# Performance work log

Hardware: AMD Instinct MI355X
Metric: run time of the kernel (lower is better)

Reference implementation:

```python
import jax, jax.numpy as jnp
import numpy as np

B, R, C, H = 2048, 100, 64, 256  # batch graphs, regions/graph, in_channels, hidden
N = B * R                         # total nodes
E = 3276800                       # edges


def setup_inputs() -> dict:
    key = jax.random.key(0)
    ks = jax.random.split(key, 12)
    state = jax.random.normal(ks[0], (N, C), dtype=jnp.float32)
    edge_index = jax.random.randint(ks[1], (2, E), 0, N, dtype=jnp.int64)
    action = jax.random.uniform(ks[2], (B, R, R), dtype=jnp.float32)
    s = lambda f: 1.0 / np.sqrt(f)
    W_gcn = jax.random.uniform(ks[3], (C, C), jnp.float32, -s(C), s(C))
    b_gcn = jnp.zeros((C,), jnp.float32)
    W1 = jax.random.uniform(ks[4], (C + R, H), jnp.float32, -s(C + R), s(C + R))
    b1 = jax.random.uniform(ks[5], (H,), jnp.float32, -s(C + R), s(C + R))
    W2 = jax.random.uniform(ks[6], (H, H), jnp.float32, -s(H), s(H))
    b2 = jax.random.uniform(ks[7], (H,), jnp.float32, -s(H), s(H))
    W3 = jax.random.uniform(ks[8], (H, 1), jnp.float32, -s(H), s(H))
    b3 = jax.random.uniform(ks[9], (1,), jnp.float32, -s(H), s(H))
    return {"state": state, "edge_index": edge_index, "action": action,
            "W_gcn": W_gcn, "b_gcn": b_gcn, "W1": W1, "b1": b1,
            "W2": W2, "b2": b2, "W3": W3, "b3": b3}


def gcn_conv(x, edge_index, W, b):
    # PyG GCNConv: add self-loops, symmetric degree normalization, then aggregate.
    n = x.shape[0]
    loops = jnp.arange(n, dtype=edge_index.dtype)
    src = jnp.concatenate([edge_index[0], loops])
    dst = jnp.concatenate([edge_index[1], loops])
    deg = jax.ops.segment_sum(jnp.ones_like(dst, dtype=x.dtype), dst, num_segments=n)
    dinv = deg ** -0.5  # deg >= 1 thanks to self-loops
    xw = x @ W
    msg = xw[src] * (dinv[src] * dinv[dst])[:, None]
    return jax.ops.segment_sum(msg, dst, num_segments=n) + b


def reference(state, edge_index, action, W_gcn, b_gcn, W1, b1, W2, b2, W3, b3):
    out = jax.nn.relu(gcn_conv(state, edge_index, W_gcn, b_gcn))
    x = out + state                              # residual, [N, C]
    x = x.reshape(-1, R, C)                      # [B, R, C]
    concat = jnp.concatenate([x, action], axis=-1)  # [B, R, C+R]
    x = jax.nn.relu(concat @ W1 + b1)
    x = jax.nn.relu(x @ W2 + b2)
    x = jnp.sum(x, axis=1)                       # sum pooling over regions -> [B, H]
    return (x @ W3 + b3).squeeze(-1)             # [B]
```

## Files before the change

### kernel.cpp

```cpp
#include <hip/hip_runtime.h>
#include <hip/hip_bf16.h>
#include <cstdint>
#include <cstddef>

#define N_NODES 204800
#define N_EDGES 3276800
#define NB 2048
#define NR 100
#define NC 64
#define NH 256
#define KPAD 192
#define NBKT 400

typedef __attribute__((ext_vector_type(8))) short short8;
typedef __attribute__((ext_vector_type(4))) float f32x4;
typedef unsigned int uint32;

__device__ __forceinline__ void gload16(const void* g, void* l) {
    __builtin_amdgcn_global_load_lds(
        (const __attribute__((address_space(1))) uint32_t*)(g),
        (__attribute__((address_space(3))) uint32_t*)(l), 16, 0, 0);
}

__device__ __forceinline__ ushort f2bf(float v) {
    __hip_bfloat16 h = __float2bfloat16(v);
    return *reinterpret_cast<ushort*>(&h);
}

__device__ __forceinline__ uint32 pack2bf(float a, float b) {
    return (uint32)f2bf(a) | ((uint32)f2bf(b) << 16);
}

__device__ __forceinline__ float bflo(uint32 v) { return __uint_as_float(v << 16); }
__device__ __forceinline__ float bfhi(uint32 v) { return __uint_as_float(v & 0xFFFF0000u); }


__global__ __launch_bounds__(256) void k_bhist(const int* __restrict__ ei,
                                               int* __restrict__ bcnt) {
    __shared__ int h[NBKT];
    int t = threadIdx.x;
    for (int i = t; i < NBKT; i += 256) h[i] = 0;
    __syncthreads();
    #pragma unroll 16
    for (int k = 0; k < 16; ++k) {
        int e = blockIdx.x * 4096 + k * 256 + t;
        atomicAdd(&h[ei[N_EDGES + e] >> 9], 1);
    }
    __syncthreads();
    for (int i = t; i < NBKT; i += 256)
        if (h[i]) atomicAdd(&bcnt[i], h[i]);
}

__global__ void k_bscan(const int* __restrict__ bcnt, int* __restrict__ boffs,
                        int* __restrict__ bcur) {
    __shared__ int tmp[512];
    int t = threadIdx.x;
    int v = (t < NBKT) ? bcnt[t] : 0;
    tmp[t] = v;
    __syncthreads();
    for (int off = 1; off < 512; off <<= 1) {
        int x = 0;
        if (t >= off) x = tmp[t - off];
        __syncthreads();
        tmp[t] += x;
        __syncthreads();
    }
    if (t < NBKT) {
        int o = tmp[t] - v;
        boffs[t] = o;
        bcur[t] = o;
    }
}

__global__ __launch_bounds__(256) void k_bscat(const int* __restrict__ ei,
                                               int* __restrict__ bcur,
                                               uint32* __restrict__ part) {
    __shared__ int hist[NBKT];
    __shared__ int curb[NBKT];
    int tid = threadIdx.x;
    for (int i = tid; i < NBKT; i += 256) hist[i] = 0;
    __syncthreads();
    #pragma unroll 16
    for (int k = 0; k < 16; ++k) {
        int e = blockIdx.x * 4096 + k * 256 + tid;
        atomicAdd(&hist[ei[N_EDGES + e] >> 9], 1);
    }
    __syncthreads();
    for (int i = tid; i < NBKT; i += 256) {
        int c = hist[i];
        curb[i] = c ? atomicAdd(&bcur[i], c) : 0;
    }
    __syncthreads();
    #pragma unroll 16
    for (int k = 0; k < 16; ++k) {
        int e = blockIdx.x * 4096 + k * 256 + tid;
        int s = ei[e];
        int d = ei[N_EDGES + e];
        int b = d >> 9;
        int p = atomicAdd(&curb[b], 1);
        part[p] = (uint32)s | ((uint32)(d & 511) << 18);
    }
}

__global__ __launch_bounds__(512) void k_sortb(
    const uint32* __restrict__ part, const int* __restrict__ boffs,
    const int* __restrict__ bcnt, int* __restrict__ csr,
    int* __restrict__ cnt, int* __restrict__ offs, float* __restrict__ dinv,
    const float* __restrict__ state, uint32* __restrict__ ssb32) {
    __shared__ int h[512];
    __shared__ int cur[512];
    __shared__ float sdv[512];
    int b = blockIdx.x, t = threadIdx.x;
    h[t] = 0;
    __syncthreads();
    int base = boffs[b], n = bcnt[b];
    for (int i = t; i < n; i += 512)
        atomicAdd(&h[part[base + i] >> 18], 1);
    __syncthreads();
    int v = h[t];
    int node = b * 512 + t;
    cnt[node] = v;
    float dv = rsqrtf((float)(v + 1));
    dinv[node] = dv;
    sdv[t] = dv;
    __syncthreads();
    for (int off = 1; off < 512; off <<= 1) {
        int x = 0;
        if (t >= off) x = h[t - off];
        __syncthreads();
        h[t] += x;
        __syncthreads();
    }
    int excl = h[t] - v;
    offs[node] = base + excl;
    cur[t] = excl;
    __syncthreads();
    for (int i = t; i < n; i += 512) {
        uint32 ew = part[base + i];
        int dl = ew >> 18;
        int pos = atomicAdd(&cur[dl], 1);
        csr[base + pos] = (int)(ew & 0x3FFFF);
    }
    __syncthreads();
    for (int i = t; i < 512 * 32; i += 512) {
        int nl = i >> 5, u = i & 31;
        float d = sdv[nl];
        size_t idx = (size_t)(b * 512 + nl) * 32 + u;
        float2 sv = reinterpret_cast<const float2*>(state)[idx];
        ssb32[idx] = pack2bf(sv.x * d, sv.y * d);
    }
}

__global__ __launch_bounds__(256) void k_gcn(
    const uint32* __restrict__ ssb32, const float* __restrict__ state,
    const int* __restrict__ csr, const int* __restrict__ offs,
    const int* __restrict__ cnt, const float* __restrict__ dinv,
    const ushort* __restrict__ Wgt, const float* __restrict__ bg,
    ushort* __restrict__ xb16) {
    __shared__ uint32 av[32 * 36];
    __shared__ ushort wgs[64 * 72];
    int tid = threadIdx.x;
    int w = tid >> 6, lane = tid & 63;
    int half = lane >> 5, l = lane & 31;
    int R0 = blockIdx.x * 32;

    {
        int r = tid >> 2, c0 = (tid & 3) * 16;
        short8 v0 = *(const short8*)(Wgt + r * 64 + c0);
        short8 v1 = *(const short8*)(Wgt + r * 64 + c0 + 8);
        *(short8*)(wgs + r * 72 + c0) = v0;
        *(short8*)(wgs + r * 72 + c0 + 8) = v1;
    }

    for (int rr = 0; rr < 4; ++rr) {
        int lrow = w * 8 + rr * 2 + half;
        int row = R0 + lrow;
        float di = dinv[row];
        float2 st2 = *reinterpret_cast<const float2*>(state + (size_t)row * 64 + 2 * l);
        int s0 = offs[row], c = cnt[row];
        float x0 = 0.f, y0 = 0.f, x1 = 0.f, y1 = 0.f;
        float x2 = 0.f, y2 = 0.f, x3 = 0.f, y3 = 0.f;
        int e = 0;
        for (; e + 8 <= c; e += 8) {
            int sa = csr[s0 + e + 0];
            int sb = csr[s0 + e + 1];
            int sc = csr[s0 + e + 2];
            int sd = csr[s0 + e + 3];
            int se = csr[s0 + e + 4];
            int sf = csr[s0 + e + 5];
            int sg = csr[s0 + e + 6];
            int sh = csr[s0 + e + 7];
            uint32 va = ssb32[(size_t)sa * 32 + l];
            uint32 vb = ssb32[(size_t)sb * 32 + l];
            uint32 vc = ssb32[(size_t)sc * 32 + l];
            uint32 vd = ssb32[(size_t)sd * 32 + l];
            uint32 ve = ssb32[(size_t)se * 32 + l];
            uint32 vf = ssb32[(size_t)sf * 32 + l];
            uint32 vg = ssb32[(size_t)sg * 32 + l];
            uint32 vh = ssb32[(size_t)sh * 32 + l];
            x0 += bflo(va); y0 += bfhi(va);
            x1 += bflo(vb); y1 += bfhi(vb);
            x2 += bflo(vc); y2 += bfhi(vc);
            x3 += bflo(vd); y3 += bfhi(vd);
            x0 += bflo(ve); y0 += bfhi(ve);
            x1 += bflo(vf); y1 += bfhi(vf);
            x2 += bflo(vg); y2 += bfhi(vg);
            x3 += bflo(vh); y3 += bfhi(vh);
        }
        for (; e + 4 <= c; e += 4) {
            int sa = csr[s0 + e + 0];
            int sb = csr[s0 + e + 1];
            int sc = csr[s0 + e + 2];
            int sd = csr[s0 + e + 3];
            uint32 va = ssb32[(size_t)sa * 32 + l];
            uint32 vb = ssb32[(size_t)sb * 32 + l];
            uint32 vc = ssb32[(size_t)sc * 32 + l];
            uint32 vd = ssb32[(size_t)sd * 32 + l];
            x0 += bflo(va); y0 += bfhi(va);
            x1 += bflo(vb); y1 += bfhi(vb);
            x2 += bflo(vc); y2 += bfhi(vc);
            x3 += bflo(vd); y3 += bfhi(vd);
        }
        for (; e < c; ++e) {
            int s = csr[s0 + e];
            uint32 v = ssb32[(size_t)s * 32 + l];
            x0 += bflo(v); y0 += bfhi(v);
        }
        float ax = ((x0 + x1) + (x2 + x3)) * di + di * di * st2.x;
        float ay = ((y0 + y1) + (y2 + y3)) * di + di * di * st2.y;
        av[lrow * 36 + l] = pack2bf(ax, ay);
    }
    __syncthreads();

    int l15 = lane & 15, l4 = lane >> 4;
    const ushort* avs = (const ushort*)av;
    f32x4 acc[2] = {};
    #pragma unroll
    for (int kk = 0; kk < 2; ++kk) {
        short8 bf = *(const short8*)(wgs + (w * 16 + l15) * 72 + kk * 32 + l4 * 8);
        #pragma unroll
        for (int mt = 0; mt < 2; ++mt) {
            short8 af = *(const short8*)(avs + (mt * 16 + l15) * 72 + kk * 32 + l4 * 8);
            acc[mt] = __builtin_amdgcn_mfma_f32_16x16x32_bf16(af, bf, acc[mt], 0, 0, 0);
        }
    }
    int col = w * 16 + l15;
    float bgv = bg[col];
    #pragma unroll
    for (int mt = 0; mt < 2; ++mt)
        #pragma unroll
        for (int r = 0; r < 4; ++r) {
            int row = R0 + mt * 16 + l4 * 4 + r;
            float v = fmaxf(acc[mt][r] + bgv, 0.f) + state[(size_t)row * 64 + col];
            xb16[(size_t)row * 64 + col] = f2bf(v);
        }
}

__global__ void k_packW(const float* __restrict__ W1, const float* __restrict__ W2,
                        const float* __restrict__ Wg, const float* __restrict__ b1,
                        ushort* __restrict__ W1f, ushort* __restrict__ W2f,
                        ushort* __restrict__ Wgt) {
    int t = blockIdx.x * 256 + threadIdx.x;
    if (t < 6 * 4 * 256 * 8) {
        int u = t & 7, chunk = t >> 3;
        int tid = chunk & 255, ktI = chunk >> 8;
        int kt = ktI >> 2, i = ktI & 3;
        int l = tid & 63, wp = tid >> 6;
        int k = kt * 32 + (l >> 4) * 8 + u;
        int j = i * 64 + wp * 16 + (l & 15);
        ushort v = 0;
        if (k < NC + NR) v = f2bf(W1[(size_t)k * NH + j]);
        else if (k == NC + NR) v = f2bf(b1[j]);
        W1f[t] = v;
    } else if (t < 49152 + 8 * 4 * 256 * 8) {
        int t2 = t - 49152;
        int u = t2 & 7, chunk = t2 >> 3;
        int tid = chunk & 255, ktI = chunk >> 8;
        int kt = ktI >> 2, i = ktI & 3;
        int l = tid & 63, wp = tid >> 6;
        int k = kt * 32 + (l >> 4) * 8 + u;
        int j = i * 64 + wp * 16 + (l & 15);
        W2f[t2] = f2bf(W2[(size_t)k * NH + j]);
    } else {
        int t3 = t - 49152 - 65536;
        if (t3 < 64 * 64) {
            int n = t3 >> 6, k = t3 & 63;
            Wgt[t3] = f2bf(Wg[(size_t)k * 64 + n]);
        }
    }
}

__global__ __launch_bounds__(512, 4) void k_mlpf(
    const ushort* __restrict__ xb16, const float* __restrict__ action,
    const ushort* __restrict__ W1f, const ushort* __restrict__ W2f,
    const float* __restrict__ b2, const float* __restrict__ W3,
    float* __restrict__ out) {
    __shared__ __align__(16) ushort Bs[2][256 * 32];
    int tid = threadIdx.x;
    int w = tid >> 6, lane = tid & 63;
    int s = lane & 15, g = lane >> 4;
    int m0 = blockIdx.x * 128;
    int myrow = m0 + w * 16 + s;
    int gb = myrow / 100, grr = myrow - gb * 100;
    const float* abp = action + (size_t)gb * 10000 + (size_t)grr * 100;

    short8 xf0 = *(const short8*)(xb16 + (size_t)myrow * 64 + g * 8);
    short8 xf1 = *(const short8*)(xb16 + (size_t)myrow * 64 + 32 + g * 8);

    #pragma unroll
    for (int tc = 0; tc < 2; ++tc)
        gload16(W1f + ((size_t)(0 * 1024 + tc * 512 + tid)) * 8,
                (char*)Bs[0] + (tc * 512 + tid) * 16);
    __syncthreads();

    f32x4 acc1[16] = {};
    float4 pa0 = {0.f, 0.f, 0.f, 0.f}, pa1 = {0.f, 0.f, 0.f, 0.f};
    int cur = 0;

    #pragma unroll
    for (int kt = 0; kt < 6; ++kt) {
        int nxt = cur ^ 1;
        short8 bf;
        if (kt == 0) bf = xf0;
        else if (kt == 1) bf = xf1;
        else if (kt < 5) {
            ushort tm[8];
            tm[0] = f2bf(pa0.x); tm[1] = f2bf(pa0.y); tm[2] = f2bf(pa0.z); tm[3] = f2bf(pa0.w);
            tm[4] = f2bf(pa1.x); tm[5] = f2bf(pa1.y); tm[6] = f2bf(pa1.z); tm[7] = f2bf(pa1.w);
            bf = *(const short8*)tm;
        } else {
            ushort tm[8];
            if (g == 0) {
                tm[0] = f2bf(pa0.x); tm[1] = f2bf(pa0.y); tm[2] = f2bf(pa0.z); tm[3] = f2bf(pa0.w);
                tm[4] = (ushort)0x3F80; tm[5] = 0; tm[6] = 0; tm[7] = 0;
            } else {
                #pragma unroll
                for (int u = 0; u < 8; ++u) tm[u] = 0;
            }
            bf = *(const short8*)tm;
        }
        if (kt >= 1 && kt <= 3) {
            int c0 = (kt + 1) * 32 - 64 + g * 8;
            pa0 = *(const float4*)(abp + c0);
            pa1 = *(const float4*)(abp + c0 + 4);
        } else if (kt == 4) {
            if (g == 0) pa0 = *(const float4*)(abp + 96);
        }
        if (kt < 5) {
            #pragma unroll
            for (int tc = 0; tc < 2; ++tc)
                gload16(W1f + ((size_t)((kt + 1) * 1024 + tc * 512 + tid)) * 8,
                        (char*)Bs[nxt] + (tc * 512 + tid) * 16);
        } else {
            #pragma unroll
            for (int tc = 0; tc < 2; ++tc)
                gload16(W2f + ((size_t)(0 * 1024 + tc * 512 + tid)) * 8,
                        (char*)Bs[nxt] + (tc * 512 + tid) * 16);
        }
        #pragma unroll
        for (int jt = 0; jt < 16; ++jt) {
            short8 af = *(const short8*)((const char*)Bs[cur] + jt * 1024 + lane * 16);
            acc1[jt] = __builtin_amdgcn_mfma_f32_16x16x32_bf16(af, bf, acc1[jt], 0, 0, 0);
        }
        __syncthreads();
        cur = nxt;
    }

    uint32 q0[16], q1[16];
    #pragma unroll
    for (int jt = 0; jt < 16; ++jt) {
        q0[jt] = pack2bf(fmaxf(acc1[jt][0], 0.f), fmaxf(acc1[jt][1], 0.f));
        q1[jt] = pack2bf(fmaxf(acc1[jt][2], 0.f), fmaxf(acc1[jt][3], 0.f));
    }

    f32x4 acc2[16] = {};
    int src0 = ((lane & 16) << 1) | s;
    int src1 = src0 + 16;
    bool hiSel = (lane & 32) != 0;
    #pragma unroll
    for (int kt = 0; kt < 8; ++kt) {
        int nxt = cur ^ 1;
        if (kt < 7) {
            #pragma unroll
            for (int tc = 0; tc < 2; ++tc)
                gload16(W2f + ((size_t)((kt + 1) * 1024 + tc * 512 + tid)) * 8,
                        (char*)Bs[nxt] + (tc * 512 + tid) * 16);
        }
        uint32 al0 = (uint32)__shfl((int)q0[2 * kt],     src0);
        uint32 ah0 = (uint32)__shfl((int)q0[2 * kt + 1], src0);
        uint32 bl0 = (uint32)__shfl((int)q1[2 * kt],     src0);
        uint32 bh0 = (uint32)__shfl((int)q1[2 * kt + 1], src0);
        uint32 al1 = (uint32)__shfl((int)q0[2 * kt],     src1);
        uint32 ah1 = (uint32)__shfl((int)q0[2 * kt + 1], src1);
        uint32 bl1 = (uint32)__shfl((int)q1[2 * kt],     src1);
        uint32 bh1 = (uint32)__shfl((int)q1[2 * kt + 1], src1);
        short8 af;
        uint32* afp = (uint32*)&af;
        afp[0] = hiSel ? ah0 : al0;
        afp[1] = hiSel ? bh0 : bl0;
        afp[2] = hiSel ? ah1 : al1;
        afp[3] = hiSel ? bh1 : bl1;
        #pragma unroll
        for (int nt = 0; nt < 16; ++nt) {
            short8 bf = *(const short8*)((const char*)Bs[cur] + nt * 1024 + lane * 16);
            acc2[nt] = __builtin_amdgcn_mfma_f32_16x16x32_bf16(af, bf, acc2[nt], 0, 0, 0);
        }
        __syncthreads();
        cur = nxt;
    }

    float vsum[4] = {0.f, 0.f, 0.f, 0.f};
    #pragma unroll
    for (int nt = 0; nt < 16; ++nt) {
        float b2v = b2[nt * 16 + s];
        float w3v = W3[nt * 16 + s];
        #pragma unroll
        for (int r = 0; r < 4; ++r)
            vsum[r] += fmaxf(acc2[nt][r] + b2v, 0.f) * w3v;
    }
    float* red = (float*)Bs;
    #pragma unroll
    for (int r = 0; r < 4; ++r) {
        float v = vsum[r];
        v += __shfl_xor(v, 1);
        v += __shfl_xor(v, 2);
        v += __shfl_xor(v, 4);
        v += __shfl_xor(v, 8);
        if (s == 0) red[w * 16 + g * 4 + r] = v;
    }
    __syncthreads();
    if (tid < 128) {
        float sv = red[tid];
        int half64 = tid >> 6;
        int lt = tid & 63;
        int gbase = m0 + half64 * 64;
        int g0 = gbase / 100;
        int r0 = gbase - g0 * 100;
        int split = 100 - r0; if (split > 64) split = 64;
        float v0 = (lt < split) ? sv : 0.f;
        float vs = sv;
        #pragma unroll
        for (int d = 1; d < 64; d <<= 1) {
            v0 += __shfl_xor(v0, d);
            vs += __shfl_xor(vs, d);
        }
        if (lt == 0) {
            atomicAdd(&out[g0], v0);
            if (split < 64) atomicAdd(&out[g0 + 1], vs - v0);
        }
    }
}

__global__ void k_init_out(float* __restrict__ out, const float* __restrict__ b3) {
    int i = blockIdx.x * 256 + threadIdx.x;
    out[i] = b3[0];
}


extern "C" void kernel_launch(void* const* d_in, const int* in_sizes, int n_in,
                              void* d_out, int out_size, void* d_ws, size_t ws_size,
                              hipStream_t stream) {
    const float* state  = (const float*)d_in[0];
    const int*   ei     = (const int*)d_in[1];
    const float* action = (const float*)d_in[2];
    const float* Wg     = (const float*)d_in[3];
    const float* bg     = (const float*)d_in[4];
    const float* W1     = (const float*)d_in[5];
    const float* b1     = (const float*)d_in[6];
    const float* W2     = (const float*)d_in[7];
    const float* b2     = (const float*)d_in[8];
    const float* W3     = (const float*)d_in[9];
    const float* b3     = (const float*)d_in[10];
    float* out = (float*)d_out;

    char* ws = (char*)d_ws;
    uint32* part  = (uint32*)(ws + 0);
    uint32* ssb32 = (uint32*)(ws + 13107200);
    ushort* xb16  = (ushort*)(ws + 39321600);
    int*   csr    = (int*)  (ws + 65536000);
    int*   cnt    = (int*)  (ws + 78643200);
    int*   offs   = (int*)  (ws + 79462400);
    float* dinv   = (float*)(ws + 80281600);
    int*   bcnt   = (int*)  (ws + 81100800);
    int*   boffs  = (int*)  (ws + 81102400);
    int*   bcur   = (int*)  (ws + 81104000);
    ushort* W1f   = (ushort*)(ws + 81105600);
    ushort* W2f   = (ushort*)(ws + 81203904);
    ushort* Wgt   = (ushort*)(ws + 81334976);

    hipMemsetAsync(bcnt, 0, NBKT * sizeof(int), stream);
    k_init_out<<<NB / 256, 256, 0, stream>>>(out, b3);

    k_bhist<<<N_EDGES / 4096, 256, 0, stream>>>(ei, bcnt);
    k_bscan<<<1, 512, 0, stream>>>(bcnt, boffs, bcur);
    k_bscat<<<N_EDGES / 4096, 256, 0, stream>>>(ei, bcur, part);
    k_sortb<<<NBKT, 512, 0, stream>>>(part, boffs, bcnt, csr, cnt, offs, dinv,
                                      state, ssb32);
    k_packW<<<(49152 + 65536 + 4096 + 255) / 256, 256, 0, stream>>>(
        W1, W2, Wg, b1, W1f, W2f, Wgt);
    k_gcn<<<N_NODES / 32, 256, 0, stream>>>(ssb32, state, csr, offs, cnt, dinv,
                                            Wgt, bg, xb16);
    k_mlpf<<<N_NODES / 128, 512, 0, stream>>>(xb16, action, W1f, W2f, b2, W3, out);
}
```

Baseline: 271.0 us.

## Fuse GCN aggregation and projection into the MLP kernel

Removes the separate k_gcn kernel and performs the CSR gather-aggregation and the 64x64 GCN matmul inside k_mlpf for each 128-row tile. The residual result is staged in shared memory as bf16 and read directly as the first MLP operand. This avoids writing and re-reading the xb16 intermediate and saves one launch. In exchange it raises shared memory use per block, which may cut occupancy, and places latency-bound gathers ahead of the MFMA-heavy MLP in the same kernel.

```diff
diff --git a/kernel.cpp b/kernel.cpp
--- a/kernel.cpp
+++ b/kernel.cpp
@@ -149,111 +149,6 @@
         float2 sv = reinterpret_cast<const float2*>(state)[idx];
         ssb32[idx] = pack2bf(sv.x * d, sv.y * d);
     }
-}
-
-__global__ __launch_bounds__(256) void k_gcn(
-    const uint32* __restrict__ ssb32, const float* __restrict__ state,
-    const int* __restrict__ csr, const int* __restrict__ offs,
-    const int* __restrict__ cnt, const float* __restrict__ dinv,
-    const ushort* __restrict__ Wgt, const float* __restrict__ bg,
-    ushort* __restrict__ xb16) {
-    __shared__ uint32 av[32 * 36];
-    __shared__ ushort wgs[64 * 72];
-    int tid = threadIdx.x;
-    int w = tid >> 6, lane = tid & 63;
-    int half = lane >> 5, l = lane & 31;
-    int R0 = blockIdx.x * 32;
-
-    {
-        int r = tid >> 2, c0 = (tid & 3) * 16;
-        short8 v0 = *(const short8*)(Wgt + r * 64 + c0);
-        short8 v1 = *(const short8*)(Wgt + r * 64 + c0 + 8);
-        *(short8*)(wgs + r * 72 + c0) = v0;
-        *(short8*)(wgs + r * 72 + c0 + 8) = v1;
-    }
-
-    for (int rr = 0; rr < 4; ++rr) {
-        int lrow = w * 8 + rr * 2 + half;
-        int row = R0 + lrow;
-        float di = dinv[row];
-        float2 st2 = *reinterpret_cast<const float2*>(state + (size_t)row * 64 + 2 * l);
-        int s0 = offs[row], c = cnt[row];
-        float x0 = 0.f, y0 = 0.f, x1 = 0.f, y1 = 0.f;
-        float x2 = 0.f, y2 = 0.f, x3 = 0.f, y3 = 0.f;
-        int e = 0;
-        for (; e + 8 <= c; e += 8) {
-            int sa = csr[s0 + e + 0];
-            int sb = csr[s0 + e + 1];
-            int sc = csr[s0 + e + 2];
-            int sd = csr[s0 + e + 3];
-            int se = csr[s0 + e + 4];
-            int sf = csr[s0 + e + 5];
-            int sg = csr[s0 + e + 6];
-            int sh = csr[s0 + e + 7];
-            uint32 va = ssb32[(size_t)sa * 32 + l];
-            uint32 vb = ssb32[(size_t)sb * 32 + l];
-            uint32 vc = ssb32[(size_t)sc * 32 + l];
-            uint32 vd = ssb32[(size_t)sd * 32 + l];
-            uint32 ve = ssb32[(size_t)se * 32 + l];
-            uint32 vf = ssb32[(size_t)sf * 32 + l];
-            uint32 vg = ssb32[(size_t)sg * 32 + l];
-            uint32 vh = ssb32[(size_t)sh * 32 + l];
-            x0 += bflo(va); y0 += bfhi(va);
-            x1 += bflo(vb); y1 += bfhi(vb);
-            x2 += bflo(vc); y2 += bfhi(vc);
-            x3 += bflo(vd); y3 += bfhi(vd);
-            x0 += bflo(ve); y0 += bfhi(ve);
-            x1 += bflo(vf); y1 += bfhi(vf);
-            x2 += bflo(vg); y2 += bfhi(vg);
-            x3 += bflo(vh); y3 += bfhi(vh);
-        }
-        for (; e + 4 <= c; e += 4) {
-            int sa = csr[s0 + e + 0];
-            int sb = csr[s0 + e + 1];
-            int sc = csr[s0 + e + 2];
-            int sd = csr[s0 + e + 3];
-            uint32 va = ssb32[(size_t)sa * 32 + l];
-            uint32 vb = ssb32[(size_t)sb * 32 + l];
-            uint32 vc = ssb32[(size_t)sc * 32 + l];
-            uint32 vd = ssb32[(size_t)sd * 32 + l];
-            x0 += bflo(va); y0 += bfhi(va);
-            x1 += bflo(vb); y1 += bfhi(vb);
-            x2 += bflo(vc); y2 += bfhi(vc);
-            x3 += bflo(vd); y3 += bfhi(vd);
-        }
-        for (; e < c; ++e) {
-            int s = csr[s0 + e];
-            uint32 v = ssb32[(size_t)s * 32 + l];
-            x0 += bflo(v); y0 += bfhi(v);
-        }
-        float ax = ((x0 + x1) + (x2 + x3)) * di + di * di * st2.x;
-        float ay = ((y0 + y1) + (y2 + y3)) * di + di * di * st2.y;
-        av[lrow * 36 + l] = pack2bf(ax, ay);
-    }
-    __syncthreads();
-
-    int l15 = lane & 15, l4 = lane >> 4;
-    const ushort* avs = (const ushort*)av;
-    f32x4 acc[2] = {};
-    #pragma unroll
-    for (int kk = 0; kk < 2; ++kk) {
-        short8 bf = *(const short8*)(wgs + (w * 16 + l15) * 72 + kk * 32 + l4 * 8);
-        #pragma unroll
-        for (int mt = 0; mt < 2; ++mt) {
-            short8 af = *(const short8*)(avs + (mt * 16 + l15) * 72 + kk * 32 + l4 * 8);
-            acc[mt] = __builtin_amdgcn_mfma_f32_16x16x32_bf16(af, bf, acc[mt], 0, 0, 0);
-        }
-    }
-    int col = w * 16 + l15;
-    float bgv = bg[col];
-    #pragma unroll
-    for (int mt = 0; mt < 2; ++mt)
-        #pragma unroll
-        for (int r = 0; r < 4; ++r) {
-            int row = R0 + mt * 16 + l4 * 4 + r;
-            float v = fmaxf(acc[mt][r] + bgv, 0.f) + state[(size_t)row * 64 + col];
-            xb16[(size_t)row * 64 + col] = f2bf(v);
-        }
 }
 
 __global__ void k_packW(const float* __restrict__ W1, const float* __restrict__ W2,
@@ -291,11 +186,18 @@
 }
 
 __global__ __launch_bounds__(512, 4) void k_mlpf(
-    const ushort* __restrict__ xb16, const float* __restrict__ action,
+    const uint32* __restrict__ ssb32, const float* __restrict__ state,
+    const int* __restrict__ csr, const int* __restrict__ offs,
+    const int* __restrict__ cnt, const float* __restrict__ dinv,
+    const ushort* __restrict__ Wgt, const float* __restrict__ bg,
+    const float* __restrict__ action,
     const ushort* __restrict__ W1f, const ushort* __restrict__ W2f,
     const float* __restrict__ b2, const float* __restrict__ W3,
     float* __restrict__ out) {
     __shared__ __align__(16) ushort Bs[2][256 * 32];
+    __shared__ __align__(16) uint32 av[128 * 36];
+    __shared__ __align__(16) ushort wgs[64 * 72];
+    __shared__ __align__(16) uint32 xs[128 * 36];
     int tid = threadIdx.x;
     int w = tid >> 6, lane = tid & 63;
     int s = lane & 15, g = lane >> 4;
@@ -304,14 +206,108 @@
     int gb = myrow / 100, grr = myrow - gb * 100;
     const float* abp = action + (size_t)gb * 10000 + (size_t)grr * 100;
 
-    short8 xf0 = *(const short8*)(xb16 + (size_t)myrow * 64 + g * 8);
-    short8 xf1 = *(const short8*)(xb16 + (size_t)myrow * 64 + 32 + g * 8);
-
     #pragma unroll
     for (int tc = 0; tc < 2; ++tc)
         gload16(W1f + ((size_t)(0 * 1024 + tc * 512 + tid)) * 8,
                 (char*)Bs[0] + (tc * 512 + tid) * 16);
-    __syncthreads();
+    {
+        int r = tid >> 3, c0 = (tid & 7) * 8;
+        *(short8*)(wgs + r * 72 + c0) = *(const short8*)(Wgt + r * 64 + c0);
+    }
+
+    {
+        int half = lane >> 5, l = lane & 31;
+        for (int rr = 0; rr < 8; ++rr) {
+            int lrow = w * 16 + rr * 2 + half;
+            int row = m0 + lrow;
+            float di = dinv[row];
+            float2 st2 = *reinterpret_cast<const float2*>(state + (size_t)row * 64 + 2 * l);
+            int s0 = offs[row], c = cnt[row];
+            float x0 = 0.f, y0 = 0.f, x1 = 0.f, y1 = 0.f;
+            float x2 = 0.f, y2 = 0.f, x3 = 0.f, y3 = 0.f;
+            int e = 0;
+            for (; e + 8 <= c; e += 8) {
+                int sa = csr[s0 + e + 0];
+                int sb = csr[s0 + e + 1];
+                int sc = csr[s0 + e + 2];
+                int sd = csr[s0 + e + 3];
+                int se = csr[s0 + e + 4];
+                int sf = csr[s0 + e + 5];
+                int sg = csr[s0 + e + 6];
+                int sh = csr[s0 + e + 7];
+                uint32 va = ssb32[(size_t)sa * 32 + l];
+                uint32 vb = ssb32[(size_t)sb * 32 + l];
+                uint32 vc = ssb32[(size_t)sc * 32 + l];
+                uint32 vd = ssb32[(size_t)sd * 32 + l];
+                uint32 ve = ssb32[(size_t)se * 32 + l];
+                uint32 vf = ssb32[(size_t)sf * 32 + l];
+                uint32 vg = ssb32[(size_t)sg * 32 + l];
+                uint32 vh = ssb32[(size_t)sh * 32 + l];
+                x0 += bflo(va); y0 += bfhi(va);
+                x1 += bflo(vb); y1 += bfhi(vb);
+                x2 += bflo(vc); y2 += bfhi(vc);
+                x3 += bflo(vd); y3 += bfhi(vd);
+                x0 += bflo(ve); y0 += bfhi(ve);
+                x1 += bflo(vf); y1 += bfhi(vf);
+                x2 += bflo(vg); y2 += bfhi(vg);
+                x3 += bflo(vh); y3 += bfhi(vh);
+            }
+            for (; e + 4 <= c; e += 4) {
+                int sa = csr[s0 + e + 0];
+                int sb = csr[s0 + e + 1];
+                int sc = csr[s0 + e + 2];
+                int sd = csr[s0 + e + 3];
+                uint32 va = ssb32[(size_t)sa * 32 + l];
+                uint32 vb = ssb32[(size_t)sb * 32 + l];
+                uint32 vc = ssb32[(size_t)sc * 32 + l];
+                uint32 vd = ssb32[(size_t)sd * 32 + l];
+                x0 += bflo(va); y0 += bfhi(va);
+                x1 += bflo(vb); y1 += bfhi(vb);
+                x2 += bflo(vc); y2 += bfhi(vc);
+                x3 += bflo(vd); y3 += bfhi(vd);
+            }
+            for (; e < c; ++e) {
+                int sv2 = csr[s0 + e];
+                uint32 v = ssb32[(size_t)sv2 * 32 + l];
+                x0 += bflo(v); y0 += bfhi(v);
+            }
+            float ax = ((x0 + x1) + (x2 + x3)) * di + di * di * st2.x;
+            float ay = ((y0 + y1) + (y2 + y3)) * di + di * di * st2.y;
+            av[lrow * 36 + l] = pack2bf(ax, ay);
+        }
+    }
+    __syncthreads();
+
+    {
+        f32x4 accx[4] = {};
+        #pragma unroll
+        for (int kk = 0; kk < 2; ++kk) {
+            short8 bfa = *(const short8*)((const char*)av +
+                          (((w * 16 + s) * 36 + kk * 16 + g * 4) << 2));
+            #pragma unroll
+            for (int jt = 0; jt < 4; ++jt) {
+                short8 af = *(const short8*)(wgs + (jt * 16 + s) * 72 + kk * 32 + g * 8);
+                accx[jt] = __builtin_amdgcn_mfma_f32_16x16x32_bf16(af, bfa, accx[jt], 0, 0, 0);
+            }
+        }
+        #pragma unroll
+        for (int jt = 0; jt < 4; ++jt) {
+            int j0 = jt * 16 + g * 4;
+            float4 bg4 = *(const float4*)(bg + j0);
+            float4 st4 = *(const float4*)(state + (size_t)myrow * 64 + j0);
+            float xv0 = fmaxf(accx[jt][0] + bg4.x, 0.f) + st4.x;
+            float xv1 = fmaxf(accx[jt][1] + bg4.y, 0.f) + st4.y;
+            float xv2 = fmaxf(accx[jt][2] + bg4.z, 0.f) + st4.z;
+            float xv3 = fmaxf(accx[jt][3] + bg4.w, 0.f) + st4.w;
+            uint32* dst = &xs[(w * 16 + s) * 36 + jt * 8 + g * 2];
+            dst[0] = pack2bf(xv0, xv1);
+            dst[1] = pack2bf(xv2, xv3);
+        }
+    }
+    __syncthreads();
+
+    short8 xf0 = *(const short8*)((const char*)xs + (((w * 16 + s) * 36 + g * 4) << 2));
+    short8 xf1 = *(const short8*)((const char*)xs + (((w * 16 + s) * 36 + 16 + g * 4) << 2));
 
     f32x4 acc1[16] = {};
     float4 pa0 = {0.f, 0.f, 0.f, 0.f}, pa1 = {0.f, 0.f, 0.f, 0.f};
@@ -476,7 +472,6 @@
     char* ws = (char*)d_ws;
     uint32* part  = (uint32*)(ws + 0);
     uint32* ssb32 = (uint32*)(ws + 13107200);
-    ushort* xb16  = (ushort*)(ws + 39321600);
     int*   csr    = (int*)  (ws + 65536000);
     int*   cnt    = (int*)  (ws + 78643200);
     int*   offs   = (int*)  (ws + 79462400);
@@ -498,7 +493,6 @@
                                       state, ssb32);
     k_packW<<<(49152 + 65536 + 4096 + 255) / 256, 256, 0, stream>>>(
         W1, W2, Wg, b1, W1f, W2f, Wgt);
-    k_gcn<<<N_NODES / 32, 256, 0, stream>>>(ssb32, state, csr, offs, cnt, dinv,
-                                            Wgt, bg, xb16);
-    k_mlpf<<<N_NODES / 128, 512, 0, stream>>>(xb16, action, W1f, W2f, b2, W3, out);
-}
+    k_mlpf<<<N_NODES / 128, 512, 0, stream>>>(ssb32, state, csr, offs, cnt, dinv,
+                                              Wgt, bg, action, W1f, W2f, b2, W3, out);
+}
```

Result: slower. 326.7 us (+20.6%).
